# Kernel tuning notes

Hardware: AMD Instinct MI355X
Metric: run time of the kernel (lower is better)

## Reference

```python
import jax, jax.numpy as jnp
import numpy as np

N_EMBED = 1024
N_HEADS = 16
HEAD_SIZE = N_EMBED // N_HEADS
BLOCK_SIZE = 256
LN_EPS = 1e-5


def _layernorm(x, g, b):
    mu = jnp.mean(x, axis=-1, keepdims=True)
    var = jnp.var(x, axis=-1, keepdims=True)
    return (x - mu) * jax.lax.rsqrt(var + LN_EPS) * g + b


def setup_inputs() -> dict:
    key = jax.random.key(0)
    ks = jax.random.split(key, 12)
    B, T, C, H, D = 64, 256, N_EMBED, N_HEADS, HEAD_SIZE
    s = lambda fan_in: 1.0 / np.sqrt(fan_in)
    return {
        "x": jax.random.normal(ks[0], (B, T, C), jnp.float32),
        # per-head Q/K/V projections (bias=False in torch), stacked over heads
        "Wq": jax.random.uniform(ks[1], (H, C, D), jnp.float32, -s(C), s(C)),
        "Wk": jax.random.uniform(ks[2], (H, C, D), jnp.float32, -s(C), s(C)),
        "Wv": jax.random.uniform(ks[3], (H, C, D), jnp.float32, -s(C), s(C)),
        "Wproj": jax.random.uniform(ks[4], (C, C), jnp.float32, -s(C), s(C)),
        "bproj": jax.random.uniform(ks[5], (C,), jnp.float32, -s(C), s(C)),
        "W1": jax.random.uniform(ks[6], (C, 4 * C), jnp.float32, -s(C), s(C)),
        "b1": jax.random.uniform(ks[7], (4 * C,), jnp.float32, -s(C), s(C)),
        "W2": jax.random.uniform(ks[8], (4 * C, C), jnp.float32, -s(4 * C), s(4 * C)),
        "b2": jax.random.uniform(ks[9], (C,), jnp.float32, -s(4 * C), s(4 * C)),
        "ln1_g": jnp.ones((C,), jnp.float32),
        "ln1_b": jnp.zeros((C,), jnp.float32),
        "ln2_g": jnp.ones((C,), jnp.float32),
        "ln2_b": jnp.zeros((C,), jnp.float32),
    }


def reference(x, Wq, Wk, Wv, Wproj, bproj, W1, b1, W2, b2, ln1_g, ln1_b, ln2_g, ln2_b):
    B, T, C = x.shape
    # --- self-attention sub-block ---
    h = _layernorm(x, ln1_g, ln1_b)
    q = jnp.einsum("btc,hcd->bhtd", h, Wq)
    k = jnp.einsum("btc,hcd->bhtd", h, Wk)
    v = jnp.einsum("btc,hcd->bhtd", h, Wv)
    # NOTE: original scales by C**-0.5 with C = n_embed (full dim), not head_size
    scores = jnp.einsum("bhtd,bhsd->bhts", q, k) * (C ** -0.5)
    causal = jnp.tril(jnp.ones((T, T), bool))
    scores = jnp.where(causal, scores, -jnp.inf)
    wei = jax.nn.softmax(scores, axis=-1)
    attn = jnp.einsum("bhts,bhsd->bhtd", wei, v)  # [B,H,T,D]
    attn = attn.transpose(0, 2, 1, 3).reshape(B, T, C)  # concat heads
    x = x + attn @ Wproj + bproj
    # --- feed-forward sub-block ---
    h2 = _layernorm(x, ln2_g, ln2_b)
    ffn = jax.nn.relu(h2 @ W1 + b1) @ W2 + b2
    return x + ffn
```

## Files before the change

kernel.cpp:

```cpp
#include <hip/hip_runtime.h>
#include <stdint.h>

using u16 = unsigned short;
using u32 = unsigned int;

typedef __attribute__((ext_vector_type(8))) short s16x8;
typedef __attribute__((ext_vector_type(4))) float f32x4;

__device__ __forceinline__ float bflo(u32 u) { u32 t = u << 16; float f; __builtin_memcpy(&f, &t, 4); return f; }
__device__ __forceinline__ float bfhi(u32 u) { u32 t = u & 0xffff0000u; float f; __builtin_memcpy(&f, &t, 4); return f; }
__device__ __forceinline__ u16 f2bf(float f) {
  u32 u; __builtin_memcpy(&u, &f, 4);
  return (u16)((u + 0x7fffu + ((u >> 16) & 1u)) >> 16);
}

__device__ __forceinline__ void gload_lds16(const void* g, void* l) {
  __builtin_amdgcn_global_load_lds((const __attribute__((address_space(1))) void*)g,
                                   (__attribute__((address_space(3))) void*)l, 16, 0, 0);
}

__global__ __launch_bounds__(256)
void transpose_pack(const float* __restrict__ in, u16* __restrict__ out,
                    int R, int Cc, long in_bs, long out_bs)
{
  __shared__ float tile[32][33];
  in  += (size_t)blockIdx.z * in_bs;
  out += (size_t)blockIdx.z * out_bs;
  const int r0 = blockIdx.x * 32, c0 = blockIdx.y * 32;
  const int tx = threadIdx.x & 31, ty = threadIdx.x >> 5;
#pragma unroll
  for (int i = 0; i < 4; ++i) {
    int r = ty + i * 8;
    tile[r][tx] = in[(size_t)(r0 + r) * Cc + c0 + tx];
  }
  __syncthreads();
#pragma unroll
  for (int i = 0; i < 4; ++i) {
    int c = ty + i * 8;
    out[(size_t)(c0 + c) * R + r0 + tx] = f2bf(tile[tx][c]);
  }
}

__global__ __launch_bounds__(256)
void ln_f32_bf16(const float* __restrict__ x, const float* __restrict__ g,
                 const float* __restrict__ bta, u16* __restrict__ out)
{
  const int row = blockIdx.x, tid = threadIdx.x;
  const float4 v = ((const float4*)(x + (size_t)row * 1024))[tid];
  float s  = v.x + v.y + v.z + v.w;
  float ss = v.x * v.x + v.y * v.y + v.z * v.z + v.w * v.w;
#pragma unroll
  for (int m = 1; m < 64; m <<= 1) {
    s  += __shfl_xor(s, m);
    ss += __shfl_xor(ss, m);
  }
  __shared__ float red[8];
  const int wave = tid >> 6, lane = tid & 63;
  if (lane == 0) { red[wave] = s; red[4 + wave] = ss; }
  __syncthreads();
  s  = red[0] + red[1] + red[2] + red[3];
  ss = red[4] + red[5] + red[6] + red[7];
  const float mu  = s * (1.f / 1024.f);
  const float var = ss * (1.f / 1024.f) - mu * mu;
  const float rs  = rsqrtf(var + 1e-5f);
  const float4 gg = ((const float4*)g)[tid];
  const float4 bb = ((const float4*)bta)[tid];
  u32 w0 = (u32)f2bf((v.x - mu) * rs * gg.x + bb.x) | ((u32)f2bf((v.y - mu) * rs * gg.y + bb.y) << 16);
  u32 w1 = (u32)f2bf((v.z - mu) * rs * gg.z + bb.z) | ((u32)f2bf((v.w - mu) * rs * gg.w + bb.w) << 16);
  u32* outp = (u32*)(out + (size_t)row * 1024 + tid * 4);
  outp[0] = w0; outp[1] = w1;
}

template <int EPI>
__global__ __launch_bounds__(512, 1)
void gemm8p(const u16* __restrict__ A, const u16* __restrict__ B, void* __restrict__ Cv,
            const float* __restrict__ bias, const float* __restrict__ resid,
            int M, int N, int K, int GM)
{
  __shared__ u16 lds[65536];
  const int NT = K >> 6;
  const int tid = threadIdx.x;
  const int lane = tid & 63, wv = tid >> 6;
  const int wr = wv >> 2, wc = wv & 3;
  const int r = lane & 15, kg = lane >> 4;

  const int nwg = gridDim.x;
  const int q = nwg >> 3;
  const int bid = blockIdx.x;
  const int sw = (bid & 7) * q + (bid >> 3);
  const int bn = sw / GM, bm = sw % GM;

  const u16* Ab = A + (size_t)bm * 256 * K;
  const u16* Bb = B + (size_t)bn * 256 * K;

  const int segx = (kg ^ ((r >> 1) & 3)) << 3;
  const int aoff = (wr * 128 + r) * 32 + segx;
  const int boff = 32768 + (wc * 64 + r) * 32 + segx;

  f32x4 acc[8][4];
#pragma unroll
  for (int m = 0; m < 8; ++m)
#pragma unroll
    for (int n = 0; n < 4; ++n) acc[m][n] = f32x4{0.f, 0.f, 0.f, 0.f};

  auto stage = [&](const u16* src, int u, int kh, int base) {
#pragma unroll
    for (int jj = 0; jj < 2; ++jj) {
      int ci = jj * 512 + tid;
      int row = ci >> 2;
      int sseg = (ci & 3) ^ ((ci >> 3) & 3);
      gload_lds16(src + (size_t)row * K + u * 64 + kh * 32 + sseg * 8, &lds[base + ci * 8]);
    }
  };

  stage(Ab, 0, 0, 0);
  stage(Bb, 0, 0, 32768);
  stage(Ab, 0, 1, 8192);
  stage(Bb, 0, 1, 32768 + 8192);
  if (NT > 1) {
    stage(Ab, 1, 0, 16384);
    stage(Bb, 1, 0, 32768 + 16384);
    asm volatile("s_waitcnt vmcnt(4)" ::: "memory");
  } else {
    asm volatile("s_waitcnt vmcnt(0)" ::: "memory");
  }
  __builtin_amdgcn_s_barrier();
  __builtin_amdgcn_sched_barrier(0);

  for (int t = 0; t < NT; ++t) {
    const int buf = t & 1;
    const int ab = buf * 16384;
    const bool s1 = (t + 1) < NT, s2 = (t + 2) < NT;
    s16x8 av[8], bv[4];

    if (s1) {
      stage(Ab, t + 1, 1, (buf ^ 1) * 16384 + 8192);
      stage(Bb, t + 1, 1, 32768 + (buf ^ 1) * 16384 + 8192);
    }
#pragma unroll
    for (int n = 0; n < 4; ++n) bv[n] = *(const s16x8*)&lds[ab + boff + n * 512];
#pragma unroll
    for (int m = 0; m < 8; ++m) av[m] = *(const s16x8*)&lds[ab + aoff + m * 512];
    __builtin_amdgcn_s_setprio(1);
#pragma unroll
    for (int m = 0; m < 8; ++m)
#pragma unroll
      for (int n = 0; n < 4; ++n)
        acc[m][n] = __builtin_amdgcn_mfma_f32_16x16x32_bf16(av[m], bv[n], acc[m][n], 0, 0, 0);
    __builtin_amdgcn_s_setprio(0);
    __builtin_amdgcn_sched_barrier(0);
    __builtin_amdgcn_s_barrier();

    if (s2) {
      stage(Ab, t + 2, 0, ab);
      stage(Bb, t + 2, 0, 32768 + ab);
    }
#pragma unroll
    for (int n = 0; n < 4; ++n) bv[n] = *(const s16x8*)&lds[ab + boff + 8192 + n * 512];
#pragma unroll
    for (int m = 0; m < 8; ++m) av[m] = *(const s16x8*)&lds[ab + aoff + 8192 + m * 512];
    __builtin_amdgcn_s_setprio(1);
#pragma unroll
    for (int m = 0; m < 8; ++m)
#pragma unroll
      for (int n = 0; n < 4; ++n)
        acc[m][n] = __builtin_amdgcn_mfma_f32_16x16x32_bf16(av[m], bv[n], acc[m][n], 0, 0, 0);
    __builtin_amdgcn_s_setprio(0);
    __builtin_amdgcn_sched_barrier(0);
    if (s2) asm volatile("s_waitcnt vmcnt(4)" ::: "memory");
    else    asm volatile("s_waitcnt vmcnt(0)" ::: "memory");
    __builtin_amdgcn_s_barrier();
  }

#pragma unroll
  for (int m = 0; m < 8; ++m) {
#pragma unroll
    for (int n = 0; n < 4; ++n) {
#pragma unroll
      for (int j = 0; j < 4; ++j) {
        int row = bm * 256 + wr * 128 + m * 16 + kg * 4 + j;
        int col = bn * 256 + wc * 64 + n * 16 + r;
        size_t idx = (size_t)row * N + col;
        float v = acc[m][n][j];
        if constexpr (EPI == 0) {
          ((u16*)Cv)[idx] = f2bf(v);
        } else if constexpr (EPI == 1) {
          ((float*)Cv)[idx] = v + bias[col] + resid[idx];
        } else if constexpr (EPI == 2) {
          ((u16*)Cv)[idx] = f2bf(fmaxf(v + bias[col], 0.f));
        } else {
          ((float*)Cv)[idx] = v + bias[col] + resid[idx];
        }
      }
    }
  }
}

__global__ __launch_bounds__(256)
void attn_mfma(const u16* __restrict__ qkv, u16* __restrict__ outc)
{
  const int bh = blockIdx.x, b = bh >> 4, h = bh & 15;
  const int tid = threadIdx.x;
  const int lane = tid & 63, w = tid >> 6;
  const int r = lane & 15, kg = lane >> 4;

  __shared__ u16 Ks[64 * 64];
  __shared__ u16 Vt[64 * 72];
  __shared__ u16 P[4][64 * 72];

  const u16* qbase = qkv + (size_t)(b * 256) * 3072 + h * 64;

  s16x8 qf[4][2];
#pragma unroll
  for (int m = 0; m < 4; ++m)
#pragma unroll
    for (int ks = 0; ks < 2; ++ks)
      qf[m][ks] = *(const s16x8*)(qbase + (size_t)(w * 64 + m * 16 + r) * 3072 + ks * 32 + kg * 8);

  f32x4 of[4][4];
  float mrun[4][4], lrun[4][4];
#pragma unroll
  for (int m = 0; m < 4; ++m) {
#pragma unroll
    for (int n = 0; n < 4; ++n) of[m][n] = f32x4{0.f, 0.f, 0.f, 0.f};
#pragma unroll
    for (int j = 0; j < 4; ++j) { mrun[m][j] = -1e30f; lrun[m][j] = 0.f; }
  }

  const float cexp = 0.03125f * 1.4426950408889634f;

  for (int kt = 0; kt < 4; ++kt) {
#pragma unroll
    for (int jj = 0; jj < 2; ++jj) {
      int ci = jj * 256 + tid;
      int key = ci >> 3, seg = ci & 7;
      int sseg = seg ^ (key & 7);
      gload_lds16(qkv + (size_t)(b * 256 + kt * 64 + key) * 3072 + 1024 + h * 64 + sseg * 8,
                  &Ks[ci * 8]);
    }
    {
      int row = tid >> 2, q = tid & 3;
      const u16* vg = qkv + (size_t)(b * 256 + kt * 64 + row) * 3072 + 2048 + h * 64 + q * 16;
      union { uint4 u[2]; u16 s[16]; } vv;
      vv.u[0] = *(const uint4*)vg;
      vv.u[1] = *(const uint4*)(vg + 8);
#pragma unroll
      for (int i = 0; i < 16; ++i)
        Vt[(q * 16 + i) * 72 + row] = vv.s[i];
    }
    __syncthreads();

    if (w >= kt) {
      f32x4 s[4][4];
#pragma unroll
      for (int m = 0; m < 4; ++m)
#pragma unroll
        for (int n = 0; n < 4; ++n) s[m][n] = f32x4{0.f, 0.f, 0.f, 0.f};
#pragma unroll
      for (int ks = 0; ks < 2; ++ks) {
        s16x8 kb[4];
#pragma unroll
        for (int n = 0; n < 4; ++n) {
          int row = n * 16 + r;
          int sseg = (ks * 4 + kg) ^ (row & 7);
          kb[n] = *(const s16x8*)&Ks[row * 64 + sseg * 8];
        }
#pragma unroll
        for (int m = 0; m < 4; ++m)
#pragma unroll
          for (int n = 0; n < 4; ++n)
            s[m][n] = __builtin_amdgcn_mfma_f32_16x16x32_bf16(qf[m][ks], kb[n], s[m][n], 0, 0, 0);
      }
      if (kt == w) {
#pragma unroll
        for (int m = 0; m < 4; ++m)
#pragma unroll
          for (int n = 0; n < 4; ++n)
#pragma unroll
            for (int j = 0; j < 4; ++j)
              if (n * 16 + r > m * 16 + kg * 4 + j) s[m][n][j] = -1e30f;
      }
#pragma unroll
      for (int m = 0; m < 4; ++m) {
        float rm[4], rsc[4], ls[4];
#pragma unroll
        for (int j = 0; j < 4; ++j) {
          rm[j] = fmaxf(fmaxf(s[m][0][j], s[m][1][j]), fmaxf(s[m][2][j], s[m][3][j]));
          rm[j] = fmaxf(rm[j], __shfl_xor(rm[j], 1));
          rm[j] = fmaxf(rm[j], __shfl_xor(rm[j], 2));
          rm[j] = fmaxf(rm[j], __shfl_xor(rm[j], 4));
          rm[j] = fmaxf(rm[j], __shfl_xor(rm[j], 8));
          float mnew = fmaxf(mrun[m][j], rm[j]);
          rsc[j] = exp2f((mrun[m][j] - mnew) * cexp);
          mrun[m][j] = mnew;
          ls[j] = 0.f;
        }
#pragma unroll
        for (int n = 0; n < 4; ++n)
#pragma unroll
          for (int j = 0; j < 4; ++j) {
            float p = exp2f((s[m][n][j] - mrun[m][j]) * cexp);
            ls[j] += p;
            P[w][(m * 16 + kg * 4 + j) * 72 + n * 16 + r] = f2bf(p);
          }
#pragma unroll
        for (int j = 0; j < 4; ++j) {
          ls[j] += __shfl_xor(ls[j], 1);
          ls[j] += __shfl_xor(ls[j], 2);
          ls[j] += __shfl_xor(ls[j], 4);
          ls[j] += __shfl_xor(ls[j], 8);
          lrun[m][j] = lrun[m][j] * rsc[j] + ls[j];
        }
#pragma unroll
        for (int n = 0; n < 4; ++n)
#pragma unroll
          for (int j = 0; j < 4; ++j)
            of[m][n][j] *= rsc[j];
      }
#pragma unroll
      for (int kk = 0; kk < 2; ++kk) {
        s16x8 pa[4], vb[4];
#pragma unroll
        for (int m = 0; m < 4; ++m)
          pa[m] = *(const s16x8*)&P[w][(m * 16 + r) * 72 + kk * 32 + kg * 8];
#pragma unroll
        for (int n = 0; n < 4; ++n)
          vb[n] = *(const s16x8*)&Vt[(n * 16 + r) * 72 + kk * 32 + kg * 8];
#pragma unroll
        for (int m = 0; m < 4; ++m)
#pragma unroll
          for (int n = 0; n < 4; ++n)
            of[m][n] = __builtin_amdgcn_mfma_f32_16x16x32_bf16(pa[m], vb[n], of[m][n], 0, 0, 0);
      }
    }
    __syncthreads();
  }

#pragma unroll
  for (int m = 0; m < 4; ++m) {
    float inv[4];
#pragma unroll
    for (int j = 0; j < 4; ++j) inv[j] = 1.f / lrun[m][j];
#pragma unroll
    for (int n = 0; n < 4; ++n)
#pragma unroll
      for (int j = 0; j < 4; ++j) {
        int row = b * 256 + w * 64 + m * 16 + kg * 4 + j;
        outc[(size_t)row * 1024 + h * 64 + n * 16 + r] = f2bf(of[m][n][j] * inv[j]);
      }
  }
}

extern "C" void kernel_launch(void* const* d_in, const int* in_sizes, int n_in,
                              void* d_out, int out_size, void* d_ws, size_t ws_size,
                              hipStream_t stream) {
  (void)in_sizes; (void)n_in; (void)out_size; (void)ws_size;
  const float* x     = (const float*)d_in[0];
  const float* Wq    = (const float*)d_in[1];
  const float* Wk    = (const float*)d_in[2];
  const float* Wv    = (const float*)d_in[3];
  const float* Wproj = (const float*)d_in[4];
  const float* bproj = (const float*)d_in[5];
  const float* W1    = (const float*)d_in[6];
  const float* b1    = (const float*)d_in[7];
  const float* W2    = (const float*)d_in[8];
  const float* b2    = (const float*)d_in[9];
  const float* ln1g  = (const float*)d_in[10];
  const float* ln1b  = (const float*)d_in[11];
  const float* ln2g  = (const float*)d_in[12];
  const float* ln2b  = (const float*)d_in[13];
  float* out = (float*)d_out;

  char* ws = (char*)d_ws;
  u16*   WqkvT  = (u16*)(ws + 0);
  u16*   WprojT = (u16*)(ws + 6291456);
  u16*   W1T    = (u16*)(ws + 8388608);
  u16*   W2T    = (u16*)(ws + 16777216);
  u16*   hb     = (u16*)(ws + 25165824);
  u16*   qkvb   = (u16*)(ws + 58720256);
  float* x2     = (float*)(ws + 159383552);
  u16*   h2     = (u16*)(ws + 226492416);
  u16*   ffn1   = (u16*)(ws + 25165824);
  u16*   attnout = hb;

  const int M = 16384;

  transpose_pack<<<dim3(32, 2, 16), 256, 0, stream>>>(Wq, WqkvT,           1024, 64, 65536, 65536);
  transpose_pack<<<dim3(32, 2, 16), 256, 0, stream>>>(Wk, WqkvT + 1048576, 1024, 64, 65536, 65536);
  transpose_pack<<<dim3(32, 2, 16), 256, 0, stream>>>(Wv, WqkvT + 2097152, 1024, 64, 65536, 65536);
  transpose_pack<<<dim3(32, 32, 1), 256, 0, stream>>>(Wproj, WprojT, 1024, 1024, 0, 0);
  transpose_pack<<<dim3(32, 128, 1), 256, 0, stream>>>(W1, W1T, 1024, 4096, 0, 0);
  transpose_pack<<<dim3(128, 32, 1), 256, 0, stream>>>(W2, W2T, 4096, 1024, 0, 0);

  ln_f32_bf16<<<M, 256, 0, stream>>>(x, ln1g, ln1b, hb);

  gemm8p<0><<<64 * 12, 512, 0, stream>>>(hb, WqkvT, qkvb, nullptr, nullptr, M, 3072, 1024, 64);

  attn_mfma<<<1024, 256, 0, stream>>>(qkvb, attnout);

  gemm8p<1><<<64 * 4, 512, 0, stream>>>(attnout, WprojT, x2, bproj, x, M, 1024, 1024, 64);

  ln_f32_bf16<<<M, 256, 0, stream>>>(x2, ln2g, ln2b, h2);

  gemm8p<2><<<64 * 16, 512, 0, stream>>>(h2, W1T, ffn1, b1, nullptr, M, 4096, 1024, 64);

  gemm8p<3><<<64 * 4, 512, 0, stream>>>(ffn1, W2T, out, b2, x2, M, 1024, 4096, 64);
}
```

Measured before the change: 650.4 us.

## Restructure GEMM LDS layout to full 64-wide K rows with inline-asm ds_reads

The GEMM main loop changes its LDS layout from two 32-wide K halves to full 64-element rows with an 8-way XOR swizzle. The three-stage half-tile prefetch becomes a plain double buffer of whole 64-K tiles, with one barrier per K step instead of two. LDS fragment reads are now inline-asm ds_read_b128 with immediate offsets, and B-tile loads are interleaved between the reads and the MFMAs. This cuts address arithmetic and barrier count, but prefetch depth drops to one tile and every iteration ends with a full vmcnt(0) wait, which may expose global latency.

```diff
diff --git a/kernel.cpp b/kernel.cpp
--- a/kernel.cpp
+++ b/kernel.cpp
@@ -93,9 +93,10 @@
   const u16* Ab = A + (size_t)bm * 256 * K;
   const u16* Bb = B + (size_t)bn * 256 * K;
 
-  const int segx = (kg ^ ((r >> 1) & 3)) << 3;
-  const int aoff = (wr * 128 + r) * 32 + segx;
-  const int boff = 32768 + (wc * 64 + r) * 32 + segx;
+  const u32 ldsb = (u32)(uintptr_t)lds;
+  const u32 segb = (u32)((kg ^ (r >> 1)) << 4);
+  const u32 abase = ldsb + (u32)((wr * 128 + r) * 128) + segb;
+  const u32 bbase = ldsb + 65536u + (u32)((wc * 64 + r) * 128) + segb;
 
   f32x4 acc[8][4];
 #pragma unroll
@@ -103,72 +104,66 @@
 #pragma unroll
     for (int n = 0; n < 4; ++n) acc[m][n] = f32x4{0.f, 0.f, 0.f, 0.f};
 
-  auto stage = [&](const u16* src, int u, int kh, int base) {
+  auto stage = [&](const u16* src, int u, int h, int base_u16) {
 #pragma unroll
     for (int jj = 0; jj < 2; ++jj) {
       int ci = jj * 512 + tid;
-      int row = ci >> 2;
-      int sseg = (ci & 3) ^ ((ci >> 3) & 3);
-      gload_lds16(src + (size_t)row * K + u * 64 + kh * 32 + sseg * 8, &lds[base + ci * 8]);
+      int rl = ci >> 3;
+      int sseg = (ci & 7) ^ ((rl >> 1) & 7);
+      gload_lds16(src + (size_t)(h * 128 + rl) * K + u * 64 + sseg * 8,
+                  &lds[base_u16 + h * 8192 + ci * 8]);
     }
   };
 
-  stage(Ab, 0, 0, 0);
-  stage(Bb, 0, 0, 32768);
-  stage(Ab, 0, 1, 8192);
-  stage(Bb, 0, 1, 32768 + 8192);
-  if (NT > 1) {
-    stage(Ab, 1, 0, 16384);
-    stage(Bb, 1, 0, 32768 + 16384);
-    asm volatile("s_waitcnt vmcnt(4)" ::: "memory");
-  } else {
-    asm volatile("s_waitcnt vmcnt(0)" ::: "memory");
-  }
+#define DSR(d, a, o) asm volatile("ds_read_b128 %0, %1 offset:" o : "=v"(d) : "v"(a))
+#define READS(aR, bR) \
+  DSR(bv0, bR, "0"); DSR(bv1, bR, "2048"); DSR(bv2, bR, "4096"); DSR(bv3, bR, "6144"); \
+  DSR(av0, aR, "0"); DSR(av1, aR, "2048"); DSR(av2, aR, "4096"); DSR(av3, aR, "6144"); \
+  DSR(av4, aR, "8192"); DSR(av5, aR, "10240"); DSR(av6, aR, "12288"); DSR(av7, aR, "14336")
+#define MM(m, n) acc[m][n] = __builtin_amdgcn_mfma_f32_16x16x32_bf16(av##m, bv##n, acc[m][n], 0, 0, 0)
+#define MFMAS() \
+  MM(0,0); MM(0,1); MM(0,2); MM(0,3); MM(1,0); MM(1,1); MM(1,2); MM(1,3); \
+  MM(2,0); MM(2,1); MM(2,2); MM(2,3); MM(3,0); MM(3,1); MM(3,2); MM(3,3); \
+  MM(4,0); MM(4,1); MM(4,2); MM(4,3); MM(5,0); MM(5,1); MM(5,2); MM(5,3); \
+  MM(6,0); MM(6,1); MM(6,2); MM(6,3); MM(7,0); MM(7,1); MM(7,2); MM(7,3)
+
+  stage(Ab, 0, 0, 0);      stage(Ab, 0, 1, 0);
+  stage(Bb, 0, 0, 32768);  stage(Bb, 0, 1, 32768);
+  asm volatile("s_waitcnt vmcnt(0)" ::: "memory");
   __builtin_amdgcn_s_barrier();
-  __builtin_amdgcn_sched_barrier(0);
 
   for (int t = 0; t < NT; ++t) {
     const int buf = t & 1;
-    const int ab = buf * 16384;
-    const bool s1 = (t + 1) < NT, s2 = (t + 2) < NT;
-    s16x8 av[8], bv[4];
-
-    if (s1) {
-      stage(Ab, t + 1, 1, (buf ^ 1) * 16384 + 8192);
-      stage(Bb, t + 1, 1, 32768 + (buf ^ 1) * 16384 + 8192);
-    }
-#pragma unroll
-    for (int n = 0; n < 4; ++n) bv[n] = *(const s16x8*)&lds[ab + boff + n * 512];
-#pragma unroll
-    for (int m = 0; m < 8; ++m) av[m] = *(const s16x8*)&lds[ab + aoff + m * 512];
-    __builtin_amdgcn_s_setprio(1);
-#pragma unroll
-    for (int m = 0; m < 8; ++m)
-#pragma unroll
-      for (int n = 0; n < 4; ++n)
-        acc[m][n] = __builtin_amdgcn_mfma_f32_16x16x32_bf16(av[m], bv[n], acc[m][n], 0, 0, 0);
-    __builtin_amdgcn_s_setprio(0);
+    const bool s1 = (t + 1) < NT;
+    const int nb = (buf ^ 1) * 16384;
+    const u32 aA0 = abase + (u32)(buf * 32768);
+    const u32 aB0 = bbase + (u32)(buf * 32768);
+    const u32 aA1 = aA0 ^ 64u;
+    const u32 aB1 = aB0 ^ 64u;
+
+    if (s1) { stage(Ab, t + 1, 0, nb); stage(Ab, t + 1, 1, nb); }
     __builtin_amdgcn_sched_barrier(0);
-    __builtin_amdgcn_s_barrier();
-
-    if (s2) {
-      stage(Ab, t + 2, 0, ab);
-      stage(Bb, t + 2, 0, 32768 + ab);
-    }
-#pragma unroll
-    for (int n = 0; n < 4; ++n) bv[n] = *(const s16x8*)&lds[ab + boff + 8192 + n * 512];
-#pragma unroll
-    for (int m = 0; m < 8; ++m) av[m] = *(const s16x8*)&lds[ab + aoff + 8192 + m * 512];
-    __builtin_amdgcn_s_setprio(1);
-#pragma unroll
-    for (int m = 0; m < 8; ++m)
-#pragma unroll
-      for (int n = 0; n < 4; ++n)
-        acc[m][n] = __builtin_amdgcn_mfma_f32_16x16x32_bf16(av[m], bv[n], acc[m][n], 0, 0, 0);
-    __builtin_amdgcn_s_setprio(0);
+    {
+      s16x8 av0, av1, av2, av3, av4, av5, av6, av7, bv0, bv1, bv2, bv3;
+      READS(aA0, aB0);
+      if (s1) { stage(Bb, t + 1, 0, 32768 + nb); stage(Bb, t + 1, 1, 32768 + nb); }
+      asm volatile("s_waitcnt lgkmcnt(0)" ::: "memory");
+      __builtin_amdgcn_sched_barrier(0);
+      __builtin_amdgcn_s_setprio(1);
+      MFMAS();
+      __builtin_amdgcn_s_setprio(0);
+    }
+    {
+      s16x8 av0, av1, av2, av3, av4, av5, av6, av7, bv0, bv1, bv2, bv3;
+      READS(aA1, aB1);
+      asm volatile("s_waitcnt lgkmcnt(0)" ::: "memory");
+      __builtin_amdgcn_sched_barrier(0);
+      __builtin_amdgcn_s_setprio(1);
+      MFMAS();
+      __builtin_amdgcn_s_setprio(0);
+    }
     __builtin_amdgcn_sched_barrier(0);
-    if (s2) asm volatile("s_waitcnt vmcnt(4)" ::: "memory");
-    else    asm volatile("s_waitcnt vmcnt(0)" ::: "memory");
+    asm volatile("s_waitcnt vmcnt(0)" ::: "memory");
     __builtin_amdgcn_s_barrier();
   }
 
@@ -194,6 +189,10 @@
       }
     }
   }
+#undef DSR
+#undef READS
+#undef MM
+#undef MFMAS
 }
 
 __global__ __launch_bounds__(256)
```

Result: faster. 614.4 us (-5.5%).
